# Kernel optimization log

Measured on AMD Instinct MI355X. Metric: run time of the kernel, lower is better.

## Reference

```python
import jax, jax.numpy as jnp
from jax import lax
import numpy as np

EPS = 1e-12  # torch F.normalize eps


def setup_inputs() -> dict:
    key = jax.random.key(0)
    ks = jax.random.split(key, 5)
    B, C, H, W = 8, 192, 128, 128
    heads = 4
    x = jax.random.normal(ks[0], (B, C, H, W), dtype=jnp.float32)
    qkv_w = jax.random.normal(ks[1], (3 * C, C), dtype=jnp.float32) * (1.0 / np.sqrt(C))
    dw_w = jax.random.normal(ks[2], (3 * C, 1, 3, 3), dtype=jnp.float32) * (1.0 / 3.0)
    proj_w = jax.random.normal(ks[3], (C, C), dtype=jnp.float32) * (1.0 / np.sqrt(C))
    temperature = jnp.ones((1, heads, 1, 1), dtype=jnp.float32)
    return {"x": x, "qkv_w": qkv_w, "dw_w": dw_w, "proj_w": proj_w,
            "temperature": temperature, "num_heads": heads}


def _l2_normalize(t):
    # matches torch F.normalize(dim=-1): x / max(||x||, eps)
    n = jnp.sqrt(jnp.sum(t * t, axis=-1, keepdims=True))
    return t / jnp.maximum(n, EPS)


def reference(x, qkv_w, dw_w, proj_w, temperature, num_heads):
    b, c, h, w = x.shape
    # 1x1 conv (no bias) == channel GEMM
    qkv = jnp.einsum('oc,bchw->bohw', qkv_w, x)
    # 3x3 depthwise conv, padding=1, groups=3c
    qkv = lax.conv_general_dilated(
        qkv, dw_w, window_strides=(1, 1), padding='SAME',
        feature_group_count=3 * c,
        dimension_numbers=('NCHW', 'OIHW', 'NCHW'))
    q, k, v = jnp.split(qkv, 3, axis=1)
    hw = h * w
    dh = c // num_heads  # per-head channel dim
    q = q.reshape(b, num_heads, dh, hw)
    k = k.reshape(b, num_heads, dh, hw)
    v = v.reshape(b, num_heads, dh, hw)
    q = _l2_normalize(q)
    k = _l2_normalize(k)
    # channel attention: [b, heads, dh, dh]
    attn = jnp.einsum('bhcn,bhdn->bhcd', q, k) * temperature
    attn = jax.nn.softmax(attn, axis=-1)
    out = jnp.einsum('bhcd,bhdn->bhcn', attn, v).reshape(b, c, h, w)
    out = jnp.einsum('oc,bchw->bohw', proj_w, out)
    return out
```

## Files before the change

### kernel.cpp

```cpp
#include <hip/hip_runtime.h>
#include <hip/hip_bf16.h>

#define CIN 192
#define C3 576
#define HWPX 16384
#define NHEADS 4
#define DH 48

typedef unsigned short ushort_t;
typedef __attribute__((ext_vector_type(8))) short bf16x8;
typedef __attribute__((ext_vector_type(4))) float f32x4;

__device__ __forceinline__ float bf2f(unsigned short u) {
    return __uint_as_float(((unsigned int)u) << 16);
}
__device__ __forceinline__ unsigned short f2bf(float f) {
    unsigned int u = __float_as_uint(f);
    unsigned int r = (u >> 16) & 1u;
    u += 0x7fffu + r;
    return (unsigned short)(u >> 16);
}
__device__ __forceinline__ void up8(uint4 a, float* o) {
    o[0] = __uint_as_float(a.x << 16); o[1] = __uint_as_float(a.x & 0xffff0000u);
    o[2] = __uint_as_float(a.y << 16); o[3] = __uint_as_float(a.y & 0xffff0000u);
    o[4] = __uint_as_float(a.z << 16); o[5] = __uint_as_float(a.z & 0xffff0000u);
    o[6] = __uint_as_float(a.w << 16); o[7] = __uint_as_float(a.w & 0xffff0000u);
}

#define ASYNC_COPY16(gptr, lptr)                                                   \
    __builtin_amdgcn_global_load_lds(                                              \
        (__attribute__((address_space(1))) void*)(gptr),                           \
        (__attribute__((address_space(3))) void*)(lptr), 16, 0, 0)

__global__ __launch_bounds__(256) void k_cvtw(const float* __restrict__ w,
                                              ushort_t* __restrict__ wb) {
    int i = (blockIdx.x * 256 + threadIdx.x) * 4;
    float4 v = *(const float4*)(w + i);
    uint2 pk;
    pk.x = (unsigned)f2bf(v.x) | ((unsigned)f2bf(v.y) << 16);
    pk.y = (unsigned)f2bf(v.z) | ((unsigned)f2bf(v.w) << 16);
    *(uint2*)(wb + i) = pk;
}

__global__ __launch_bounds__(512) void k_gemm(const float* __restrict__ A,
                                              const ushort_t* __restrict__ B,
                                              ushort_t* __restrict__ C) {
    __shared__ ushort_t sA[6 * 128 * 32];
    __shared__ ushort_t sB[2][192 * 32];
    const int t = threadIdx.x;
    const int lane = t & 63, wave = t >> 6;
    const int wrow = wave >> 1, wcol = wave & 1;
    const int pix0 = blockIdx.x * 128;
    const int b = blockIdx.z;

    const int cc = t >> 4;
    const int jj = t & 15;

    {
        float avf[6][8];
#pragma unroll
        for (int c = 0; c < 6; ++c) {
            const float* Ab = A + (size_t)b * CIN * HWPX +
                              (size_t)(c * 32 + cc) * HWPX + pix0 + jj;
#pragma unroll
            for (int i = 0; i < 8; ++i) avf[c][i] = Ab[16 * i];
        }
#pragma unroll
        for (int c = 0; c < 6; ++c) {
            ushort_t* s = &sA[c * 4096];
#pragma unroll
            for (int i = 0; i < 8; ++i) {
                int row = jj + 16 * i;
                int slot = ((cc >> 3) + (row >> 1) + (row >> 3)) & 3;
                s[row * 32 + slot * 8 + (cc & 7)] = f2bf(avf[c][i]);
            }
        }
    }

    auto stageB = [&](int buf, int og, int kc) {
        const ushort_t* Bb = B + (size_t)og * 192 * CIN;
        {
            int row = t >> 2, slot = t & 3;
            int g = (slot + (row >> 1)) & 3;
            const ushort_t* gp = Bb + (size_t)row * CIN + kc + g * 8;
            ushort_t* lp = &sB[buf][(wave * 64) * 8];
            ASYNC_COPY16(gp, lp);
        }
        if (t < 256) {
            int e = 512 + t;
            int row = e >> 2, slot = e & 3;
            int g = (slot + (row >> 1)) & 3;
            const ushort_t* gp = Bb + (size_t)row * CIN + kc + g * 8;
            ushort_t* lp = &sB[buf][(512 + wave * 64) * 8];
            ASYNC_COPY16(gp, lp);
        }
    };

    f32x4 acc[2][6];
#pragma unroll
    for (int mi = 0; mi < 2; ++mi)
#pragma unroll
        for (int ni = 0; ni < 6; ++ni) acc[mi][ni] = (f32x4){0.f, 0.f, 0.f, 0.f};

    stageB(0, 0, 0);

    const int ocol = lane & 15;
    const int prow = (lane >> 4) * 4;
    const int c = lane >> 4;

#pragma unroll
    for (int og = 0; og < 3; ++og) {
#pragma unroll
        for (int ks = 0; ks < 6; ++ks) {
            const int step = og * 6 + ks;
            const int buf = step & 1;
            __syncthreads();
            if (step + 1 < 18)
                stageB(buf ^ 1, (step + 1) / 6, ((step + 1) % 6) * 32);
            const ushort_t* a_ = &sA[ks * 4096];
            const ushort_t* b_ = sB[buf];
            bf16x8 af[2], bfr[6];
#pragma unroll
            for (int mi = 0; mi < 2; ++mi) {
                int row = wrow * 32 + mi * 16 + (lane & 15);
                int slot = (c + (row >> 1) + (row >> 3)) & 3;
                af[mi] = *(const bf16x8*)&a_[row * 32 + slot * 8];
            }
#pragma unroll
            for (int ni = 0; ni < 6; ++ni) {
                int row = wcol * 96 + ni * 16 + (lane & 15);
                int slot = (c - (row >> 1)) & 3;
                bfr[ni] = *(const bf16x8*)&b_[row * 32 + slot * 8];
            }
#pragma unroll
            for (int mi = 0; mi < 2; ++mi)
#pragma unroll
                for (int ni = 0; ni < 6; ++ni)
                    acc[mi][ni] = __builtin_amdgcn_mfma_f32_16x16x32_bf16(
                        af[mi], bfr[ni], acc[mi][ni], 0, 0, 0);
        }
#pragma unroll
        for (int mi = 0; mi < 2; ++mi) {
            int pix = pix0 + wrow * 32 + mi * 16 + prow;
#pragma unroll
            for (int ni = 0; ni < 6; ++ni) {
                int o = og * 192 + wcol * 96 + ni * 16 + ocol;
                f32x4 v = acc[mi][ni];
                ushort_t* Cp = C + ((size_t)b * C3 + o) * HWPX + pix;
                uint2 pk;
                pk.x = (unsigned)f2bf(v[0]) | ((unsigned)f2bf(v[1]) << 16);
                pk.y = (unsigned)f2bf(v[2]) | ((unsigned)f2bf(v[3]) << 16);
                *(uint2*)Cp = pk;
                acc[mi][ni] = (f32x4){0.f, 0.f, 0.f, 0.f};
            }
        }
    }
}

__global__ __launch_bounds__(256, 1) void k_gramdw(const ushort_t* __restrict__ pre,
                                                   const float* __restrict__ dww,
                                                   float* __restrict__ gpart,
                                                   float* __restrict__ normp) {
    __shared__ char smem[NHEADS * DH * DH * 4];
    ushort_t* sCw = (ushort_t*)smem + (threadIdx.x >> 6) * (96 * 40);
    float* sG = (float*)smem;

    const int chunk = blockIdx.x, h = blockIdx.y, b = blockIdx.z;
    const int t = threadIdx.x;
    const int lane = t & 63, wave = t >> 6;
    const int y0 = chunk * 16;

    const ushort_t* plane[3];
    float wreg[3][9];
    int pxb[3];
#pragma unroll
    for (int u = 0; u < 3; ++u) {
        int id = lane + 64 * u;
        int c96 = id >> 1;
        int gch = (c96 < DH) ? (h * DH + c96) : (CIN + h * DH + (c96 - DH));
        plane[u] = pre + ((size_t)b * C3 + gch) * HWPX;
        pxb[u] = wave * 32 + (id & 1) * 16;
#pragma unroll
        for (int k = 0; k < 9; ++k) wreg[u][k] = dww[gch * 9 + k];
    }

    float ssq[3] = {0.f, 0.f, 0.f};
    f32x4 acc[3][3];
#pragma unroll
    for (int i = 0; i < 3; ++i)
#pragma unroll
        for (int j = 0; j < 3; ++j) acc[i][j] = (f32x4){0.f, 0.f, 0.f, 0.f};

    uint4 ring[3][3][2];
    ushort_t lfr[3][3], rgr[3][3];
    uint4 nx[3][2];
    ushort_t nlf[3], nrg[3];

    auto LOADROW = [&](int YY) {
#pragma unroll
        for (int u = 0; u < 3; ++u) {
            bool ok = ((unsigned)YY < 128u);
            const ushort_t* rp = plane[u] + YY * 128 + pxb[u];
            if (ok) {
                nx[u][0] = *(const uint4*)rp;
                nx[u][1] = *(const uint4*)(rp + 8);
                nlf[u] = (pxb[u] > 0) ? rp[-1] : (ushort_t)0;
                nrg[u] = (pxb[u] + 16 < 128) ? rp[16] : (ushort_t)0;
            } else {
                nx[u][0] = make_uint4(0, 0, 0, 0);
                nx[u][1] = make_uint4(0, 0, 0, 0);
                nlf[u] = 0;
                nrg[u] = 0;
            }
        }
    };
    auto PUT = [&](int rp) {
#pragma unroll
        for (int u = 0; u < 3; ++u) {
            ring[rp][u][0] = nx[u][0];
            ring[rp][u][1] = nx[u][1];
            lfr[rp][u] = nlf[u];
            rgr[rp][u] = nrg[u];
        }
    };

    LOADROW(y0 - 1); PUT(0);
    LOADROW(y0);     PUT(1);
    LOADROW(y0 + 1); PUT(2);

    for (int s = 0; s < 16; ++s) {
        if (s < 15) LOADROW(y0 + s + 2);
#pragma unroll
        for (int u = 0; u < 3; ++u) {
            int id = lane + 64 * u;
            float in[3][18];
#pragma unroll
            for (int r = 0; r < 3; ++r) {
                in[r][0] = bf2f(lfr[r][u]);
                up8(ring[r][u][0], &in[r][1]);
                up8(ring[r][u][1], &in[r][9]);
                in[r][17] = bf2f(rgr[r][u]);
            }
            unsigned pk[8];
#pragma unroll
            for (int j2 = 0; j2 < 8; ++j2) {
                float o0 = 0.f, o1 = 0.f;
#pragma unroll
                for (int ky = 0; ky < 3; ++ky) {
                    o0 = fmaf(wreg[u][ky * 3 + 0], in[ky][2 * j2 + 0], o0);
                    o0 = fmaf(wreg[u][ky * 3 + 1], in[ky][2 * j2 + 1], o0);
                    o0 = fmaf(wreg[u][ky * 3 + 2], in[ky][2 * j2 + 2], o0);
                    o1 = fmaf(wreg[u][ky * 3 + 0], in[ky][2 * j2 + 1], o1);
                    o1 = fmaf(wreg[u][ky * 3 + 1], in[ky][2 * j2 + 2], o1);
                    o1 = fmaf(wreg[u][ky * 3 + 2], in[ky][2 * j2 + 3], o1);
                }
                ssq[u] = fmaf(o0, o0, ssq[u]);
                ssq[u] = fmaf(o1, o1, ssq[u]);
                pk[j2] = (unsigned)f2bf(o0) | ((unsigned)f2bf(o1) << 16);
            }
            uint4* dst = (uint4*)&sCw[(id >> 1) * 40 + ((id & 1) << 4)];
            dst[0] = make_uint4(pk[0], pk[1], pk[2], pk[3]);
            dst[1] = make_uint4(pk[4], pk[5], pk[6], pk[7]);
        }
        {
            bf16x8 af[3], bk[3];
#pragma unroll
            for (int i = 0; i < 3; ++i)
                af[i] = *(const bf16x8*)&sCw[(i * 16 + (lane & 15)) * 40 + (lane >> 4) * 8];
#pragma unroll
            for (int j = 0; j < 3; ++j)
                bk[j] = *(const bf16x8*)&sCw[(48 + j * 16 + (lane & 15)) * 40 + (lane >> 4) * 8];
#pragma unroll
            for (int i = 0; i < 3; ++i)
#pragma unroll
                for (int j = 0; j < 3; ++j)
                    acc[i][j] = __builtin_amdgcn_mfma_f32_16x16x32_bf16(af[i], bk[j],
                                                                        acc[i][j], 0, 0, 0);
        }
        if (s < 15) {
#pragma unroll
            for (int u = 0; u < 3; ++u) {
                ring[0][u][0] = ring[1][u][0]; ring[0][u][1] = ring[1][u][1];
                ring[1][u][0] = ring[2][u][0]; ring[1][u][1] = ring[2][u][1];
                ring[2][u][0] = nx[u][0];      ring[2][u][1] = nx[u][1];
                lfr[0][u] = lfr[1][u]; lfr[1][u] = lfr[2][u]; lfr[2][u] = nlf[u];
                rgr[0][u] = rgr[1][u]; rgr[1][u] = rgr[2][u]; rgr[2][u] = nrg[u];
            }
        }
    }

    __syncthreads();
    const int crow = (lane >> 4) * 4;
    const int dcol = lane & 15;
#pragma unroll
    for (int i = 0; i < 3; ++i)
#pragma unroll
        for (int j = 0; j < 3; ++j)
#pragma unroll
            for (int r = 0; r < 4; ++r)
                sG[(size_t)wave * DH * DH + (i * 16 + crow + r) * DH + j * 16 + dcol] =
                    acc[i][j][r];
    __syncthreads();
    float* g = gpart + (((size_t)(b * NHEADS + h)) * 8 + chunk) * (DH * DH);
    for (int e = t; e < DH * DH; e += 256)
        g[e] = sG[e] + sG[DH * DH + e] + sG[2 * DH * DH + e] + sG[3 * DH * DH + e];

    float* np = normp + ((((size_t)(b * NHEADS + h)) * 8 + chunk) * 4 + wave) * 192;
#pragma unroll
    for (int u = 0; u < 3; ++u) np[lane + 64 * u] = ssq[u];
}

__global__ __launch_bounds__(256) void k_attn(const float* __restrict__ gpart,
                                              const float* __restrict__ normp,
                                              const float* __restrict__ temperature,
                                              float* __restrict__ att) {
    __shared__ float sA[DH][DH + 1];
    __shared__ float nrm[96];
    const int h = blockIdx.x, b = blockIdx.y;
    const int t = threadIdx.x;
    const size_t bh = b * NHEADS + h;
    if (t < 96) {
        float s = 0.f;
        for (int ck = 0; ck < 8; ++ck)
#pragma unroll
            for (int w = 0; w < 4; ++w) {
                const float* np = normp + ((bh * 8 + ck) * 4 + w) * 192 + t * 2;
                s += np[0] + np[1];
            }
        nrm[t] = fmaxf(sqrtf(s), 1e-12f);
    }
    __syncthreads();
    const float* base = gpart + (bh * 8) * (DH * DH);
    for (int e = t; e < DH * DH; e += 256) {
        float s = 0.f;
#pragma unroll
        for (int c8 = 0; c8 < 8; ++c8) s += base[(size_t)c8 * DH * DH + e];
        int c = e / DH, d = e % DH;
        sA[c][d] = s / (nrm[c] * nrm[48 + d]) * temperature[h];
    }
    __syncthreads();
    if (t < DH) {
        float m = -1e30f;
#pragma unroll
        for (int d = 0; d < DH; ++d) m = fmaxf(m, sA[t][d]);
        float s = 0.f;
        float row[DH];
#pragma unroll
        for (int d = 0; d < DH; ++d) {
            row[d] = expf(sA[t][d] - m);
            s += row[d];
        }
        float inv = 1.f / s;
#pragma unroll
        for (int d = 0; d < DH; ++d) sA[t][d] = row[d] * inv;
    }
    __syncthreads();
    float* ob = att + bh * DH * DH;
    for (int e = t; e < DH * DH; e += 256) ob[e] = sA[e / DH][e % DH];
}

__global__ __launch_bounds__(256) void k_mw(const float* __restrict__ att,
                                            const float* __restrict__ proj_w,
                                            ushort_t* __restrict__ Mw) {
    __shared__ float satt[NHEADS][DH][DH];
    __shared__ float sproj[32][CIN];
    const int o0 = blockIdx.x * 32, b = blockIdx.y;
    const int t = threadIdx.x;
    {
        const float4* src = (const float4*)(att + (size_t)b * NHEADS * DH * DH);
        float4* dst = (float4*)&satt[0][0][0];
        for (int e = t; e < NHEADS * DH * DH / 4; e += 256) dst[e] = src[e];
        const float4* ps = (const float4*)(proj_w + (size_t)o0 * CIN);
        float4* pd = (float4*)&sproj[0][0];
        for (int e = t; e < 32 * CIN / 4; e += 256) pd[e] = ps[e];
    }
    __syncthreads();
    ushort_t* ob = Mw + (size_t)b * CIN * CIN + (size_t)o0 * CIN;
    for (int e = t; e < 32 * CIN; e += 256) {
        int o = e / CIN, dg = e % CIN;
        int h = dg / DH, d = dg % DH;
        float s = 0.f;
#pragma unroll
        for (int c = 0; c < DH; ++c) s = fmaf(sproj[o][h * DH + c], satt[h][c][d], s);
        ob[e] = f2bf(s);
    }
}

__global__ __launch_bounds__(512) void k_gemmv(const ushort_t* __restrict__ pre,
                                               const float* __restrict__ dww,
                                               const ushort_t* __restrict__ B,
                                               float* __restrict__ C) {
    __shared__ ushort_t sA[2][128 * 32];
    __shared__ ushort_t sB[2][192 * 32];
    const int t = threadIdx.x;
    const int lane = t & 63, wave = t >> 6;
    const int wrow = wave >> 1, wcol = wave & 1;
    const int Y = blockIdx.x;
    const int pix0 = Y * 128;
    const int b = blockIdx.z;
    const ushort_t* Bb = B + (size_t)b * CIN * CIN;

    const int cc = t >> 4;
    const int jj = t & 15;
    const int x0 = jj * 8;

    uint4 m[3];
    ushort_t l16[3], rg16[3];
    float wv[9];
    ushort_t av[8];

    auto loadV = [&](int kc) {
        int ch = kc + cc;
        const ushort_t* pl = pre + ((size_t)b * C3 + 2 * CIN + ch) * HWPX;
#pragma unroll
        for (int r = 0; r < 3; ++r) {
            int YY = Y - 1 + r;
            bool ok = ((unsigned)YY < 128u);
            const ushort_t* rp = pl + YY * 128;
            if (ok) {
                m[r] = *(const uint4*)(rp + x0);
                l16[r] = (x0 > 0) ? rp[x0 - 1] : (ushort_t)0;
                rg16[r] = (x0 < 120) ? rp[x0 + 8] : (ushort_t)0;
            } else {
                m[r] = make_uint4(0, 0, 0, 0);
                l16[r] = 0;
                rg16[r] = 0;
            }
        }
#pragma unroll
        for (int k = 0; k < 9; ++k) wv[k] = dww[(2 * CIN + ch) * 9 + k];
    };
    auto convV = [&]() {
        float in[3][10];
#pragma unroll
        for (int r = 0; r < 3; ++r) {
            in[r][0] = bf2f(l16[r]);
            up8(m[r], &in[r][1]);
            in[r][9] = bf2f(rg16[r]);
        }
#pragma unroll
        for (int j = 0; j < 8; ++j) {
            float o = 0.f;
#pragma unroll
            for (int ky = 0; ky < 3; ++ky) {
                o = fmaf(wv[ky * 3 + 0], in[ky][j + 0], o);
                o = fmaf(wv[ky * 3 + 1], in[ky][j + 1], o);
                o = fmaf(wv[ky * 3 + 2], in[ky][j + 2], o);
            }
            av[j] = f2bf(o);
        }
    };
    auto writeA = [&](int buf) {
        ushort_t* s = sA[buf];
#pragma unroll
        for (int i = 0; i < 8; ++i) {
            int row = jj * 8 + i;
            int slot = ((cc >> 3) + (row >> 1) + (row >> 3)) & 3;
            s[row * 32 + slot * 8 + (cc & 7)] = av[i];
        }
    };
    auto stageB = [&](int buf, int kc) {
        {
            int row = t >> 2, slot = t & 3;
            int g = (slot + (row >> 1)) & 3;
            const ushort_t* gp = Bb + (size_t)row * CIN + kc + g * 8;
            ushort_t* lp = &sB[buf][(wave * 64) * 8];
            ASYNC_COPY16(gp, lp);
        }
        if (t < 256) {
            int e = 512 + t;
            int row = e >> 2, slot = e & 3;
            int g = (slot + (row >> 1)) & 3;
            const ushort_t* gp = Bb + (size_t)row * CIN + kc + g * 8;
            ushort_t* lp = &sB[buf][(512 + wave * 64) * 8];
            ASYNC_COPY16(gp, lp);
        }
    };

    f32x4 acc[2][6];
#pragma unroll
    for (int mi = 0; mi < 2; ++mi)
#pragma unroll
        for (int ni = 0; ni < 6; ++ni) acc[mi][ni] = (f32x4){0.f, 0.f, 0.f, 0.f};

    loadV(0);
    convV();
    writeA(0);
    stageB(0, 0);
#pragma unroll
    for (int ks = 0; ks < 6; ++ks) {
        __syncthreads();
        const int buf = ks & 1;
        if (ks < 5) {
            loadV((ks + 1) * 32);
            stageB(buf ^ 1, (ks + 1) * 32);
        }
        const ushort_t* a_ = sA[buf];
        const ushort_t* b_ = sB[buf];
        const int c = lane >> 4;
        bf16x8 af[2], bfr[6];
#pragma unroll
        for (int mi = 0; mi < 2; ++mi) {
            int row = wrow * 32 + mi * 16 + (lane & 15);
            int slot = (c + (row >> 1) + (row >> 3)) & 3;
            af[mi] = *(const bf16x8*)&a_[row * 32 + slot * 8];
        }
#pragma unroll
        for (int ni = 0; ni < 6; ++ni) {
            int row = wcol * 96 + ni * 16 + (lane & 15);
            int slot = (c - (row >> 1)) & 3;
            bfr[ni] = *(const bf16x8*)&b_[row * 32 + slot * 8];
        }
#pragma unroll
        for (int mi = 0; mi < 2; ++mi)
#pragma unroll
            for (int ni = 0; ni < 6; ++ni)
                acc[mi][ni] = __builtin_amdgcn_mfma_f32_16x16x32_bf16(
                    af[mi], bfr[ni], acc[mi][ni], 0, 0, 0);
        if (ks < 5) {
            convV();
            writeA(buf ^ 1);
        }
    }

    const int ocol = lane & 15;
    const int prow = (lane >> 4) * 4;
#pragma unroll
    for (int mi = 0; mi < 2; ++mi) {
        int pix = pix0 + wrow * 32 + mi * 16 + prow;
#pragma unroll
        for (int ni = 0; ni < 6; ++ni) {
            int o = wcol * 96 + ni * 16 + ocol;
            f32x4 v = acc[mi][ni];
            float* Cp = C + ((size_t)b * CIN + o) * HWPX + pix;
            *(float4*)Cp = make_float4(v[0], v[1], v[2], v[3]);
        }
    }
}

extern "C" void kernel_launch(void* const* d_in, const int* in_sizes, int n_in,
                              void* d_out, int out_size, void* d_ws, size_t ws_size,
                              hipStream_t stream) {
    const float* x = (const float*)d_in[0];
    const float* qkv_w = (const float*)d_in[1];
    const float* dw_w = (const float*)d_in[2];
    const float* proj_w = (const float*)d_in[3];
    const float* temperature = (const float*)d_in[4];
    float* out = (float*)d_out;

    char* ws = (char*)d_ws;
    ushort_t* pre = (ushort_t*)ws;
    float* normp = (float*)(ws + 150994944);
    float* gpart = (float*)(ws + 151781376);
    ushort_t* Mw = (ushort_t*)(ws + 154140672);
    float* attb = (float*)(ws + 154730496);
    ushort_t* wq = (ushort_t*)(ws + 155025408);

    k_cvtw<<<dim3(108), 256, 0, stream>>>(qkv_w, wq);
    k_gemm<<<dim3(128, 1, 8), 512, 0, stream>>>(x, wq, pre);
    k_gramdw<<<dim3(8, NHEADS, 8), 256, 0, stream>>>(pre, dw_w, gpart, normp);
    k_attn<<<dim3(NHEADS, 8), 256, 0, stream>>>(gpart, normp, temperature, attb);
    k_mw<<<dim3(6, 8), 256, 0, stream>>>(attb, proj_w, Mw);
    k_gemmv<<<dim3(128, 1, 8), 512, 0, stream>>>(pre, dw_w, Mw, out);
}
```

Measured before the change: 212.7 us.

## Pre-swizzle weights into MFMA fragment layout and load B directly from global

Weight-conversion and Mw kernels now write bf16 weights in a fragment-packed order so each lane can load its MFMA B operand as one contiguous 16-byte global read. The GEMM kernels drop the LDS staging and double-buffered async copies for B. k_gemmv also stages all six K-chunks of the convolved V tile into LDS up front instead of pipelining them. This removes the per-step barriers and LDS traffic for B, but relies on L1/L2 cache hits for the weight reads, gives up compute/load overlap in k_gemmv, and raises its LDS use, which may lower occupancy.

```diff
diff --git a/kernel.cpp b/kernel.cpp
--- a/kernel.cpp
+++ b/kernel.cpp
@@ -27,98 +27,70 @@
     o[6] = __uint_as_float(a.w << 16); o[7] = __uint_as_float(a.w & 0xffff0000u);
 }
 
-#define ASYNC_COPY16(gptr, lptr)                                                   \
-    __builtin_amdgcn_global_load_lds(                                              \
-        (__attribute__((address_space(1))) void*)(gptr),                           \
-        (__attribute__((address_space(3))) void*)(lptr), 16, 0, 0)
-
 __global__ __launch_bounds__(256) void k_cvtw(const float* __restrict__ w,
                                               ushort_t* __restrict__ wb) {
     int i = (blockIdx.x * 256 + threadIdx.x) * 4;
     float4 v = *(const float4*)(w + i);
+    int row = i / CIN, k = i % CIN;
+    int og = row / 192, rowin = row % 192;
+    int ni16 = rowin >> 4, r = rowin & 15;
+    int ks = k >> 5, c = (k >> 3) & 3, e8 = k & 7;
+    size_t idx = ((((size_t)(og * 6 + ks)) * 12 + ni16) * 64 + (c * 16 + r)) * 8 + e8;
     uint2 pk;
     pk.x = (unsigned)f2bf(v.x) | ((unsigned)f2bf(v.y) << 16);
     pk.y = (unsigned)f2bf(v.z) | ((unsigned)f2bf(v.w) << 16);
-    *(uint2*)(wb + i) = pk;
+    *(uint2*)(wb + idx) = pk;
 }
 
 __global__ __launch_bounds__(512) void k_gemm(const float* __restrict__ A,
                                               const ushort_t* __restrict__ B,
                                               ushort_t* __restrict__ C) {
     __shared__ ushort_t sA[6 * 128 * 32];
-    __shared__ ushort_t sB[2][192 * 32];
     const int t = threadIdx.x;
     const int lane = t & 63, wave = t >> 6;
     const int wrow = wave >> 1, wcol = wave & 1;
     const int pix0 = blockIdx.x * 128;
     const int b = blockIdx.z;
-
     const int cc = t >> 4;
     const int jj = t & 15;
 
     {
         float avf[6][8];
 #pragma unroll
-        for (int c = 0; c < 6; ++c) {
+        for (int c6 = 0; c6 < 6; ++c6) {
             const float* Ab = A + (size_t)b * CIN * HWPX +
-                              (size_t)(c * 32 + cc) * HWPX + pix0 + jj;
-#pragma unroll
-            for (int i = 0; i < 8; ++i) avf[c][i] = Ab[16 * i];
-        }
-#pragma unroll
-        for (int c = 0; c < 6; ++c) {
-            ushort_t* s = &sA[c * 4096];
+                              (size_t)(c6 * 32 + cc) * HWPX + pix0 + jj;
+#pragma unroll
+            for (int i = 0; i < 8; ++i) avf[c6][i] = Ab[16 * i];
+        }
+#pragma unroll
+        for (int c6 = 0; c6 < 6; ++c6) {
+            ushort_t* s = &sA[c6 * 4096];
 #pragma unroll
             for (int i = 0; i < 8; ++i) {
                 int row = jj + 16 * i;
                 int slot = ((cc >> 3) + (row >> 1) + (row >> 3)) & 3;
-                s[row * 32 + slot * 8 + (cc & 7)] = f2bf(avf[c][i]);
-            }
-        }
-    }
-
-    auto stageB = [&](int buf, int og, int kc) {
-        const ushort_t* Bb = B + (size_t)og * 192 * CIN;
-        {
-            int row = t >> 2, slot = t & 3;
-            int g = (slot + (row >> 1)) & 3;
-            const ushort_t* gp = Bb + (size_t)row * CIN + kc + g * 8;
-            ushort_t* lp = &sB[buf][(wave * 64) * 8];
-            ASYNC_COPY16(gp, lp);
-        }
-        if (t < 256) {
-            int e = 512 + t;
-            int row = e >> 2, slot = e & 3;
-            int g = (slot + (row >> 1)) & 3;
-            const ushort_t* gp = Bb + (size_t)row * CIN + kc + g * 8;
-            ushort_t* lp = &sB[buf][(512 + wave * 64) * 8];
-            ASYNC_COPY16(gp, lp);
-        }
-    };
-
-    f32x4 acc[2][6];
-#pragma unroll
-    for (int mi = 0; mi < 2; ++mi)
-#pragma unroll
-        for (int ni = 0; ni < 6; ++ni) acc[mi][ni] = (f32x4){0.f, 0.f, 0.f, 0.f};
-
-    stageB(0, 0, 0);
-
+                s[row * 32 + slot * 8 + (cc & 7)] = f2bf(avf[c6][i]);
+            }
+        }
+    }
+    __syncthreads();
+
+    const int c = lane >> 4;
     const int ocol = lane & 15;
     const int prow = (lane >> 4) * 4;
-    const int c = lane >> 4;
+
+    f32x4 acc[2][6];
+#pragma unroll
+    for (int mi = 0; mi < 2; ++mi)
+#pragma unroll
+        for (int ni = 0; ni < 6; ++ni) acc[mi][ni] = (f32x4){0.f, 0.f, 0.f, 0.f};
 
 #pragma unroll
     for (int og = 0; og < 3; ++og) {
 #pragma unroll
         for (int ks = 0; ks < 6; ++ks) {
-            const int step = og * 6 + ks;
-            const int buf = step & 1;
-            __syncthreads();
-            if (step + 1 < 18)
-                stageB(buf ^ 1, (step + 1) / 6, ((step + 1) % 6) * 32);
             const ushort_t* a_ = &sA[ks * 4096];
-            const ushort_t* b_ = sB[buf];
             bf16x8 af[2], bfr[6];
 #pragma unroll
             for (int mi = 0; mi < 2; ++mi) {
@@ -128,9 +100,8 @@
             }
 #pragma unroll
             for (int ni = 0; ni < 6; ++ni) {
-                int row = wcol * 96 + ni * 16 + (lane & 15);
-                int slot = (c - (row >> 1)) & 3;
-                bfr[ni] = *(const bf16x8*)&b_[row * 32 + slot * 8];
+                size_t fidx = ((((size_t)(og * 6 + ks)) * 12 + wcol * 6 + ni) * 64 + lane) * 8;
+                bfr[ni] = *(const bf16x8*)&B[fidx];
             }
 #pragma unroll
             for (int mi = 0; mi < 2; ++mi)
@@ -375,43 +346,44 @@
         for (int e = t; e < 32 * CIN / 4; e += 256) pd[e] = ps[e];
     }
     __syncthreads();
-    ushort_t* ob = Mw + (size_t)b * CIN * CIN + (size_t)o0 * CIN;
+    ushort_t* ob = Mw + (size_t)b * CIN * CIN;
     for (int e = t; e < 32 * CIN; e += 256) {
         int o = e / CIN, dg = e % CIN;
         int h = dg / DH, d = dg % DH;
         float s = 0.f;
 #pragma unroll
         for (int c = 0; c < DH; ++c) s = fmaf(sproj[o][h * DH + c], satt[h][c][d], s);
-        ob[e] = f2bf(s);
+        int row = o0 + o;
+        int ni16 = row >> 4, r = row & 15;
+        int ks = dg >> 5, cq = (dg >> 3) & 3, e8 = dg & 7;
+        size_t idx = (((size_t)ks * 12 + ni16) * 64 + (cq * 16 + r)) * 8 + e8;
+        ob[idx] = f2bf(s);
     }
 }
 
 __global__ __launch_bounds__(512) void k_gemmv(const ushort_t* __restrict__ pre,
                                                const float* __restrict__ dww,
-                                               const ushort_t* __restrict__ B,
+                                               const ushort_t* __restrict__ Bp,
                                                float* __restrict__ C) {
-    __shared__ ushort_t sA[2][128 * 32];
-    __shared__ ushort_t sB[2][192 * 32];
+    __shared__ ushort_t sA[6 * 128 * 32];
     const int t = threadIdx.x;
     const int lane = t & 63, wave = t >> 6;
     const int wrow = wave >> 1, wcol = wave & 1;
     const int Y = blockIdx.x;
     const int pix0 = Y * 128;
     const int b = blockIdx.z;
-    const ushort_t* Bb = B + (size_t)b * CIN * CIN;
+    const ushort_t* Bb = Bp + (size_t)b * CIN * CIN;
 
     const int cc = t >> 4;
     const int jj = t & 15;
     const int x0 = jj * 8;
 
-    uint4 m[3];
-    ushort_t l16[3], rg16[3];
-    float wv[9];
-    ushort_t av[8];
-
-    auto loadV = [&](int kc) {
-        int ch = kc + cc;
+#pragma unroll
+    for (int c6 = 0; c6 < 6; ++c6) {
+        int ch = c6 * 32 + cc;
         const ushort_t* pl = pre + ((size_t)b * C3 + 2 * CIN + ch) * HWPX;
+        uint4 m[3];
+        ushort_t l16[3], rg16[3];
 #pragma unroll
         for (int r = 0; r < 3; ++r) {
             int YY = Y - 1 + r;
@@ -427,10 +399,9 @@
                 rg16[r] = 0;
             }
         }
+        float wv[9];
 #pragma unroll
         for (int k = 0; k < 9; ++k) wv[k] = dww[(2 * CIN + ch) * 9 + k];
-    };
-    auto convV = [&]() {
         float in[3][10];
 #pragma unroll
         for (int r = 0; r < 3; ++r) {
@@ -438,6 +409,7 @@
             up8(m[r], &in[r][1]);
             in[r][9] = bf2f(rg16[r]);
         }
+        ushort_t* s = &sA[c6 * 4096];
 #pragma unroll
         for (int j = 0; j < 8; ++j) {
             float o = 0.f;
@@ -447,57 +419,23 @@
                 o = fmaf(wv[ky * 3 + 1], in[ky][j + 1], o);
                 o = fmaf(wv[ky * 3 + 2], in[ky][j + 2], o);
             }
-            av[j] = f2bf(o);
-        }
-    };
-    auto writeA = [&](int buf) {
-        ushort_t* s = sA[buf];
-#pragma unroll
-        for (int i = 0; i < 8; ++i) {
-            int row = jj * 8 + i;
+            int row = jj * 8 + j;
             int slot = ((cc >> 3) + (row >> 1) + (row >> 3)) & 3;
-            s[row * 32 + slot * 8 + (cc & 7)] = av[i];
-        }
-    };
-    auto stageB = [&](int buf, int kc) {
-        {
-            int row = t >> 2, slot = t & 3;
-            int g = (slot + (row >> 1)) & 3;
-            const ushort_t* gp = Bb + (size_t)row * CIN + kc + g * 8;
-            ushort_t* lp = &sB[buf][(wave * 64) * 8];
-            ASYNC_COPY16(gp, lp);
-        }
-        if (t < 256) {
-            int e = 512 + t;
-            int row = e >> 2, slot = e & 3;
-            int g = (slot + (row >> 1)) & 3;
-            const ushort_t* gp = Bb + (size_t)row * CIN + kc + g * 8;
-            ushort_t* lp = &sB[buf][(512 + wave * 64) * 8];
-            ASYNC_COPY16(gp, lp);
-        }
-    };
-
+            s[row * 32 + slot * 8 + (cc & 7)] = f2bf(o);
+        }
+    }
+    __syncthreads();
+
+    const int c = lane >> 4;
     f32x4 acc[2][6];
 #pragma unroll
     for (int mi = 0; mi < 2; ++mi)
 #pragma unroll
         for (int ni = 0; ni < 6; ++ni) acc[mi][ni] = (f32x4){0.f, 0.f, 0.f, 0.f};
 
-    loadV(0);
-    convV();
-    writeA(0);
-    stageB(0, 0);
 #pragma unroll
     for (int ks = 0; ks < 6; ++ks) {
-        __syncthreads();
-        const int buf = ks & 1;
-        if (ks < 5) {
-            loadV((ks + 1) * 32);
-            stageB(buf ^ 1, (ks + 1) * 32);
-        }
-        const ushort_t* a_ = sA[buf];
-        const ushort_t* b_ = sB[buf];
-        const int c = lane >> 4;
+        const ushort_t* a_ = &sA[ks * 4096];
         bf16x8 af[2], bfr[6];
 #pragma unroll
         for (int mi = 0; mi < 2; ++mi) {
@@ -507,9 +445,8 @@
         }
 #pragma unroll
         for (int ni = 0; ni < 6; ++ni) {
-            int row = wcol * 96 + ni * 16 + (lane & 15);
-            int slot = (c - (row >> 1)) & 3;
-            bfr[ni] = *(const bf16x8*)&b_[row * 32 + slot * 8];
+            size_t fidx = (((size_t)ks * 12 + wcol * 6 + ni) * 64 + lane) * 8;
+            bfr[ni] = *(const bf16x8*)&Bb[fidx];
         }
 #pragma unroll
         for (int mi = 0; mi < 2; ++mi)
@@ -517,10 +454,6 @@
             for (int ni = 0; ni < 6; ++ni)
                 acc[mi][ni] = __builtin_amdgcn_mfma_f32_16x16x32_bf16(
                     af[mi], bfr[ni], acc[mi][ni], 0, 0, 0);
-        if (ks < 5) {
-            convV();
-            writeA(buf ^ 1);
-        }
     }
 
     const int ocol = lane & 15;
```

Result: no change. 211.2 us (-0.7%).
